# Kernel optimization log

Hardware: AMD Instinct MI355X
Metric: run time of the kernel (lower is better)

Reference implementation:

```python
import jax, jax.numpy as jnp
import numpy as np

# Conv config matching init_kwargs
C_IN, C_OUT = 128, 256
KH, KW = 3, 3
STRIDE = (1, 1)
PADDING = ((1, 1), (1, 1))
DILATION = (1, 1)
B, H, W = 32, 56, 56


def setup_inputs() -> dict:
    key = jax.random.key(0)
    k1, k2, k3 = jax.random.split(key, 3)
    x = jax.random.normal(k1, (B, C_IN, H, W), dtype=jnp.float32)
    # Flattened weight as stored by Conv2DUF: conv.weight.view(O,-1).t() -> [C*kh*kw, O]
    weight = jax.random.normal(k2, (C_IN * KH * KW, C_OUT), dtype=jnp.float32) * 0.02
    bias = jax.random.normal(k3, (C_OUT,), dtype=jnp.float32) * 0.02
    return {"x": x, "weight": weight, "bias": bias}


def reference(x, weight, bias):
    # Conv2DUF computes unfold(x) @ weight + bias, which is exactly a 2D
    # cross-correlation with the original conv kernel. Recover the [O,C,kh,kw]
    # kernel from the flattened [C*kh*kw, O] matrix and use the fused conv
    # primitive (same math, no giant im2col buffer).
    kernel = weight.T.reshape(C_OUT, C_IN, KH, KW)
    out = jax.lax.conv_general_dilated(
        x, kernel,
        window_strides=STRIDE,
        padding=PADDING,
        rhs_dilation=DILATION,
        dimension_numbers=("NCHW", "OIHW", "NCHW"),
    )
    return out + bias[None, :, None, None]
```

## Files before the change

### kernel.cpp

```cpp
#include <hip/hip_runtime.h>
#include <stdint.h>


#define C_INQ 128
#define C_OUTQ 256
#define HDIM 56
#define WDIM 56
#define BDIM 32
#define HP 58
#define WP 58
#define HWPIX (HDIM * WDIM)
#define GSTRIDE (BDIM * HP * WP * 8)
#define XT_ELEMS ((size_t)16 * GSTRIDE)
#define XT_BYTES (XT_ELEMS * 2)

typedef __bf16 bf16x8 __attribute__((ext_vector_type(8)));
typedef unsigned short ushort8 __attribute__((ext_vector_type(8)));
typedef float floatx4 __attribute__((ext_vector_type(4)));

__device__ __forceinline__ unsigned short f2bf(float f) {
  union { float f; unsigned int u; } v; v.f = f;
  unsigned int u = v.u;
  unsigned int r = u + 0x7FFFu + ((u >> 16) & 1u);
  return (unsigned short)(r >> 16);
}
__device__ __forceinline__ unsigned int pack2(float a, float b) {
  return (unsigned int)f2bf(a) | ((unsigned int)f2bf(b) << 16);
}

#define PAD_BLOCKS (BDIM * HP)
__global__ __launch_bounds__(256) void prep_kernel(
    const float* __restrict__ x, unsigned short* __restrict__ xt,
    const float* __restrict__ w, unsigned short* __restrict__ wt) {
  const int t = threadIdx.x;
  if (blockIdx.x < PAD_BLOCKS) {
    const int blk = blockIdx.x;
    const int b = blk / HP;
    const int hp = blk - b * HP;
    uint4* __restrict__ xt4 = (uint4*)xt;
    if (hp == 0 || hp == HP - 1) {
      for (int i = t; i < 16 * WP; i += 256) {
        int g = i / WP, wp = i - g * WP;
        xt4[((size_t)(g * BDIM + b) * HP + hp) * WP + wp] = make_uint4(0, 0, 0, 0);
      }
      return;
    }
    const int h = hp - 1;
    if (t < 224) {
      const int g = t / 14;
      const int w4 = (t - g * 14) * 4;
      const float* xp = x + ((size_t)b * C_INQ + g * 8) * HWPIX + h * WDIM + w4;
      float4 L0 = *(const float4*)(xp);
      float4 L1 = *(const float4*)(xp + HWPIX);
      float4 L2 = *(const float4*)(xp + 2 * HWPIX);
      float4 L3 = *(const float4*)(xp + 3 * HWPIX);
      float4 L4 = *(const float4*)(xp + 4 * HWPIX);
      float4 L5 = *(const float4*)(xp + 5 * HWPIX);
      float4 L6 = *(const float4*)(xp + 6 * HWPIX);
      float4 L7 = *(const float4*)(xp + 7 * HWPIX);
      uint4* dst = xt4 + ((size_t)(g * BDIM + b) * HP + hp) * WP + 1 + w4;
      dst[0] = make_uint4(pack2(L0.x, L1.x), pack2(L2.x, L3.x),
                          pack2(L4.x, L5.x), pack2(L6.x, L7.x));
      dst[1] = make_uint4(pack2(L0.y, L1.y), pack2(L2.y, L3.y),
                          pack2(L4.y, L5.y), pack2(L6.y, L7.y));
      dst[2] = make_uint4(pack2(L0.z, L1.z), pack2(L2.z, L3.z),
                          pack2(L4.z, L5.z), pack2(L6.z, L7.z));
      dst[3] = make_uint4(pack2(L0.w, L1.w), pack2(L2.w, L3.w),
                          pack2(L4.w, L5.w), pack2(L6.w, L7.w));
    } else {
      const int r = t - 224;
      const int g = r >> 1;
      const int wp = (r & 1) * (WP - 1);
      xt4[((size_t)(g * BDIM + b) * HP + hp) * WP + wp] = make_uint4(0, 0, 0, 0);
    }
  } else {
    const int bx = blockIdx.x - PAD_BLOCKS;
    const int khw = bx >> 4;
    const int r4 = bx & 15;
    const int n0w = (r4 >> 2) * 64;
    const int c32 = (r4 & 3) * 32;
    __shared__ float lds[32 * 66];
#pragma unroll
    for (int r = 0; r < 8; ++r) {
      int idx = r * 256 + t;
      int n = idx & 63, c = idx >> 6;
      lds[c * 66 + n] = w[(size_t)((c32 + c) * 9 + khw) * C_OUTQ + n0w + n];
    }
    __syncthreads();
    {
      int n = t >> 2, c8 = (t & 3) * 8;
      const float* s = lds + c8 * 66 + n;
      uint4 o;
      o.x = pack2(s[0],   s[66]);
      o.y = pack2(s[132], s[198]);
      o.z = pack2(s[264], s[330]);
      o.w = pack2(s[396], s[462]);
      *(uint4*)(wt + (size_t)khw * (C_OUTQ * C_INQ) + (size_t)(n0w + n) * C_INQ + c32 + c8) = o;
    }
  }
}

#define BM 256
#define BN 256
#define BK 64
#define NT 18

__global__ __launch_bounds__(512, 2) void conv_gemm_kernel(
    const unsigned short* __restrict__ xt,
    const unsigned short* __restrict__ wt,
    const float* __restrict__ bias,
    float* __restrict__ out) {
  __shared__ __align__(16) unsigned short ldsA[2 * BM * BK];
  __shared__ __align__(16) unsigned short ldsB[2 * BN * BK];

  const int t = threadIdx.x;
  const int lane = t & 63;
  const int wave = t >> 6;
  const int tile_m = blockIdx.x;

  int gbaseA[4], gbaseB[4];
#pragma unroll
  for (int r = 0; r < 4; ++r) {
    int g = r * 512 + t;
    int row = g >> 3;
    int kpart = (g & 7) ^ (row & 7);
    int pix = tile_m * BM + row;
    int b = pix / HWPIX;
    int p = pix - b * HWPIX;
    int h = p / WDIM;
    int w = p - h * WDIM;
    gbaseA[r] = kpart * GSTRIDE + ((b * HP + h) * WP + w) * 8;
  }
#pragma unroll
  for (int r = 0; r < 4; ++r) {
    int g = r * 512 + t;
    int n = g >> 3;
    int kpart = (g & 7) ^ (n & 7);
    gbaseB[r] = n * C_INQ + kpart * 8;
  }

  const int wm = (wave >> 2) * 128;
  const int wn = (wave & 3) * 64;
  const int mrow = lane & 15;
  const int quad = lane >> 4;
  const int xorv = mrow & 7;
  const int kx0 = (quad ^ xorv) * 8;
  const int kx1 = ((4 + quad) ^ xorv) * 8;

  floatx4 acc[8][4] = {};

  auto stage = [&](int kt, int buf) {
    const int khw = kt >> 1;
    const int chalf = kt & 1;
    const int kh = khw / 3;
    const int kw = khw - kh * 3;
    const int koffA = chalf * 8 * GSTRIDE + (kh * WP + kw) * 8;
    const int koffB = khw * (C_OUTQ * C_INQ) + chalf * 64;
    const int ldst = t * 8;
#pragma unroll
    for (int r = 0; r < 4; ++r)
      __builtin_amdgcn_global_load_lds(
          (const __attribute__((address_space(1))) unsigned int*)(xt + gbaseA[r] + koffA),
          (__attribute__((address_space(3))) unsigned int*)(ldsA + buf * (BM * BK) + r * 4096 + ldst),
          16, 0, 0);
#pragma unroll
    for (int r = 0; r < 4; ++r)
      __builtin_amdgcn_global_load_lds(
          (const __attribute__((address_space(1))) unsigned int*)(wt + gbaseB[r] + koffB),
          (__attribute__((address_space(3))) unsigned int*)(ldsB + buf * (BN * BK) + r * 4096 + ldst),
          16, 0, 0);
  };

  auto compute_tile = [&](int buf) {
    const unsigned short* A = ldsA + buf * (BM * BK);
    const unsigned short* B = ldsB + buf * (BN * BK);
    bf16x8 bfr[4][2];
#pragma unroll
    for (int j = 0; j < 4; ++j) {
      const unsigned short* br = B + (wn + j * 16 + mrow) * BK;
      bfr[j][0] = __builtin_bit_cast(bf16x8, *(const ushort8*)(br + kx0));
      bfr[j][1] = __builtin_bit_cast(bf16x8, *(const ushort8*)(br + kx1));
    }
#pragma unroll
    for (int p = 0; p < 4; ++p) {
      bf16x8 af[2][2];
#pragma unroll
      for (int i2 = 0; i2 < 2; ++i2) {
        const unsigned short* ar = A + (wm + (p * 2 + i2) * 16 + mrow) * BK;
        af[i2][0] = __builtin_bit_cast(bf16x8, *(const ushort8*)(ar + kx0));
        af[i2][1] = __builtin_bit_cast(bf16x8, *(const ushort8*)(ar + kx1));
      }
      __builtin_amdgcn_s_setprio(1);
#pragma unroll
      for (int i2 = 0; i2 < 2; ++i2)
#pragma unroll
        for (int u = 0; u < 2; ++u)
#pragma unroll
          for (int j = 0; j < 4; ++j)
            acc[p * 2 + i2][j] = __builtin_amdgcn_mfma_f32_16x16x32_bf16(
                af[i2][u], bfr[j][u], acc[p * 2 + i2][j], 0, 0, 0);
      __builtin_amdgcn_s_setprio(0);
    }
  };

#define K_STEP(T, BUF, VM, DOSTAGE)                                  \
  {                                                                  \
    asm volatile("s_waitcnt vmcnt(" VM ")" ::: "memory");            \
    __builtin_amdgcn_s_barrier();                                    \
    compute_tile(BUF);                                               \
    __builtin_amdgcn_s_barrier();                                    \
    if (DOSTAGE) stage((T) + 2, BUF);                                \
  }

  stage(0, 0);
  stage(1, 1);

#pragma unroll 1
  for (int tt = 0; tt < 16; tt += 2) {
    K_STEP(tt, 0, "8", true);
    K_STEP(tt + 1, 1, "8", true);
  }
  K_STEP(16, 0, "8", false);
  K_STEP(17, 1, "0", false);
#undef K_STEP

  float bv[4];
#pragma unroll
  for (int j = 0; j < 4; ++j) bv[j] = bias[wn + j * 16 + mrow];
#pragma unroll
  for (int i = 0; i < 8; ++i) {
    const int mbase = tile_m * BM + wm + i * 16 + quad * 4;
    const int b = mbase / HWPIX;
    const int p = mbase - b * HWPIX;
    float* obase = out + (size_t)b * (C_OUTQ * HWPIX) + p;
#pragma unroll
    for (int j = 0; j < 4; ++j) {
      const int ng = wn + j * 16 + mrow;
      floatx4 v = acc[i][j];
      v[0] += bv[j]; v[1] += bv[j]; v[2] += bv[j]; v[3] += bv[j];
      *(floatx4*)(obase + (size_t)ng * HWPIX) = v;
    }
  }
}

extern "C" void kernel_launch(void* const* d_in, const int* in_sizes, int n_in,
                              void* d_out, int out_size, void* d_ws, size_t ws_size,
                              hipStream_t stream) {
  const float* x    = (const float*)d_in[0];
  const float* w    = (const float*)d_in[1];
  const float* bias = (const float*)d_in[2];
  float* out = (float*)d_out;

  unsigned short* xt = (unsigned short*)d_ws;
  unsigned short* wt = (unsigned short*)((char*)d_ws + XT_BYTES);

  hipLaunchKernelGGL(prep_kernel, dim3(PAD_BLOCKS + 144), dim3(256), 0, stream,
                     x, xt, w, wt);
  hipLaunchKernelGGL(conv_gemm_kernel, dim3(392), dim3(512), 0, stream,
                     xt, wt, bias, out);
}
```

Before: 232.1 us.

## Rewrite conv GEMM with 128x256 tiles, 32x32 MFMA, single-buffered LDS

The GEMM kernel is restructured to use 128x256 block tiles with 256 threads and 32x32x16 bf16 MFMA instead of 16x16x32, doubling the grid to 784 blocks. Double-buffered LDS with explicit vmcnt pipelining is replaced by a single buffer synchronised with __syncthreads each K step. Block indices are remapped to interleave tiles. The aim is more blocks for occupancy and fewer MFMA instructions, at the cost of losing the load/compute overlap that double buffering gave.

```diff
diff --git a/kernel.cpp b/kernel.cpp
--- a/kernel.cpp
+++ b/kernel.cpp
@@ -17,6 +17,7 @@
 typedef __bf16 bf16x8 __attribute__((ext_vector_type(8)));
 typedef unsigned short ushort8 __attribute__((ext_vector_type(8)));
 typedef float floatx4 __attribute__((ext_vector_type(4)));
+typedef float floatx16 __attribute__((ext_vector_type(16)));
 
 __device__ __forceinline__ unsigned short f2bf(float f) {
   union { float f; unsigned int u; } v; v.f = f;
@@ -100,145 +101,120 @@
   }
 }
 
-#define BM 256
+#define BM 128
 #define BN 256
 #define BK 64
-#define NT 18
-
-__global__ __launch_bounds__(512, 2) void conv_gemm_kernel(
+#define STEPS 18
+
+__global__ __launch_bounds__(256, 2) void conv_gemm_kernel(
     const unsigned short* __restrict__ xt,
     const unsigned short* __restrict__ wt,
     const float* __restrict__ bias,
     float* __restrict__ out) {
-  __shared__ __align__(16) unsigned short ldsA[2 * BM * BK];
-  __shared__ __align__(16) unsigned short ldsB[2 * BN * BK];
+  __shared__ __align__(16) unsigned short ldsA[BM * BK];
+  __shared__ __align__(16) unsigned short ldsB[BN * BK];
 
   const int t = threadIdx.x;
   const int lane = t & 63;
   const int wave = t >> 6;
-  const int tile_m = blockIdx.x;
-
-  int gbaseA[4], gbaseB[4];
+  const int tile_m = ((int)blockIdx.x & 7) * 98 + ((int)blockIdx.x >> 3);
+
+  int gbaseA[4], gbaseB[8];
 #pragma unroll
   for (int r = 0; r < 4; ++r) {
-    int g = r * 512 + t;
+    int g = r * 256 + t;
     int row = g >> 3;
-    int kpart = (g & 7) ^ (row & 7);
+    int kp = (g & 7) ^ (row & 7);
     int pix = tile_m * BM + row;
     int b = pix / HWPIX;
     int p = pix - b * HWPIX;
     int h = p / WDIM;
     int w = p - h * WDIM;
-    gbaseA[r] = kpart * GSTRIDE + ((b * HP + h) * WP + w) * 8;
-  }
-#pragma unroll
-  for (int r = 0; r < 4; ++r) {
-    int g = r * 512 + t;
-    int n = g >> 3;
-    int kpart = (g & 7) ^ (n & 7);
-    gbaseB[r] = n * C_INQ + kpart * 8;
-  }
-
-  const int wm = (wave >> 2) * 128;
-  const int wn = (wave & 3) * 64;
-  const int mrow = lane & 15;
-  const int quad = lane >> 4;
-  const int xorv = mrow & 7;
-  const int kx0 = (quad ^ xorv) * 8;
-  const int kx1 = ((4 + quad) ^ xorv) * 8;
-
-  floatx4 acc[8][4] = {};
-
-  auto stage = [&](int kt, int buf) {
-    const int khw = kt >> 1;
-    const int chalf = kt & 1;
+    gbaseA[r] = kp * GSTRIDE + ((b * HP + h) * WP + w) * 8;
+  }
+#pragma unroll
+  for (int r = 0; r < 8; ++r) {
+    int g = r * 256 + t;
+    int row = g >> 3;
+    int kp = (g & 7) ^ (row & 7);
+    gbaseB[r] = row * C_INQ + kp * 8;
+  }
+
+  const int wm = (wave >> 1) * 64;
+  const int wn = (wave & 1) * 128;
+  const int l31 = lane & 31;
+  const int khalf = lane >> 5;
+
+  int arow[2], brow[4], sk[4];
+#pragma unroll
+  for (int mt = 0; mt < 2; ++mt) arow[mt] = (wm + mt * 32 + l31) * BK;
+#pragma unroll
+  for (int nt = 0; nt < 4; ++nt) brow[nt] = (wn + nt * 32 + l31) * BK;
+#pragma unroll
+  for (int ks = 0; ks < 4; ++ks) sk[ks] = ((2 * ks + khalf) ^ (l31 & 7)) * 8;
+
+  floatx16 acc[2][4] = {};
+
+#define BC8(p) __builtin_bit_cast(bf16x8, *(const ushort8*)(p))
+
+#pragma unroll 1
+  for (int s = 0; s < STEPS; ++s) {
+    const int khw = s >> 1;
+    const int ch = s & 1;
     const int kh = khw / 3;
     const int kw = khw - kh * 3;
-    const int koffA = chalf * 8 * GSTRIDE + (kh * WP + kw) * 8;
-    const int koffB = khw * (C_OUTQ * C_INQ) + chalf * 64;
-    const int ldst = t * 8;
+    const int koffA = ch * 8 * GSTRIDE + (kh * WP + kw) * 8;
+    const int koffB = khw * (C_OUTQ * C_INQ) + ch * 64;
 #pragma unroll
     for (int r = 0; r < 4; ++r)
       __builtin_amdgcn_global_load_lds(
           (const __attribute__((address_space(1))) unsigned int*)(xt + gbaseA[r] + koffA),
-          (__attribute__((address_space(3))) unsigned int*)(ldsA + buf * (BM * BK) + r * 4096 + ldst),
+          (__attribute__((address_space(3))) unsigned int*)(ldsA + (r * 256 + wave * 64) * 8),
           16, 0, 0);
 #pragma unroll
-    for (int r = 0; r < 4; ++r)
+    for (int r = 0; r < 8; ++r)
       __builtin_amdgcn_global_load_lds(
           (const __attribute__((address_space(1))) unsigned int*)(wt + gbaseB[r] + koffB),
-          (__attribute__((address_space(3))) unsigned int*)(ldsB + buf * (BN * BK) + r * 4096 + ldst),
+          (__attribute__((address_space(3))) unsigned int*)(ldsB + (r * 256 + wave * 64) * 8),
           16, 0, 0);
-  };
-
-  auto compute_tile = [&](int buf) {
-    const unsigned short* A = ldsA + buf * (BM * BK);
-    const unsigned short* B = ldsB + buf * (BN * BK);
-    bf16x8 bfr[4][2];
-#pragma unroll
-    for (int j = 0; j < 4; ++j) {
-      const unsigned short* br = B + (wn + j * 16 + mrow) * BK;
-      bfr[j][0] = __builtin_bit_cast(bf16x8, *(const ushort8*)(br + kx0));
-      bfr[j][1] = __builtin_bit_cast(bf16x8, *(const ushort8*)(br + kx1));
-    }
-#pragma unroll
-    for (int p = 0; p < 4; ++p) {
-      bf16x8 af[2][2];
-#pragma unroll
-      for (int i2 = 0; i2 < 2; ++i2) {
-        const unsigned short* ar = A + (wm + (p * 2 + i2) * 16 + mrow) * BK;
-        af[i2][0] = __builtin_bit_cast(bf16x8, *(const ushort8*)(ar + kx0));
-        af[i2][1] = __builtin_bit_cast(bf16x8, *(const ushort8*)(ar + kx1));
+    __syncthreads();
+
+#pragma unroll
+    for (int ks = 0; ks < 4; ++ks) {
+      bf16x8 a0 = BC8(ldsA + arow[0] + sk[ks]);
+      bf16x8 a1 = BC8(ldsA + arow[1] + sk[ks]);
+#pragma unroll
+      for (int nt = 0; nt < 4; ++nt) {
+        bf16x8 bfr = BC8(ldsB + brow[nt] + sk[ks]);
+        acc[0][nt] = __builtin_amdgcn_mfma_f32_32x32x16_bf16(a0, bfr, acc[0][nt], 0, 0, 0);
+        acc[1][nt] = __builtin_amdgcn_mfma_f32_32x32x16_bf16(a1, bfr, acc[1][nt], 0, 0, 0);
       }
-      __builtin_amdgcn_s_setprio(1);
-#pragma unroll
-      for (int i2 = 0; i2 < 2; ++i2)
-#pragma unroll
-        for (int u = 0; u < 2; ++u)
-#pragma unroll
-          for (int j = 0; j < 4; ++j)
-            acc[p * 2 + i2][j] = __builtin_amdgcn_mfma_f32_16x16x32_bf16(
-                af[i2][u], bfr[j][u], acc[p * 2 + i2][j], 0, 0, 0);
-      __builtin_amdgcn_s_setprio(0);
-    }
-  };
-
-#define K_STEP(T, BUF, VM, DOSTAGE)                                  \
-  {                                                                  \
-    asm volatile("s_waitcnt vmcnt(" VM ")" ::: "memory");            \
-    __builtin_amdgcn_s_barrier();                                    \
-    compute_tile(BUF);                                               \
-    __builtin_amdgcn_s_barrier();                                    \
-    if (DOSTAGE) stage((T) + 2, BUF);                                \
-  }
-
-  stage(0, 0);
-  stage(1, 1);
-
-#pragma unroll 1
-  for (int tt = 0; tt < 16; tt += 2) {
-    K_STEP(tt, 0, "8", true);
-    K_STEP(tt + 1, 1, "8", true);
-  }
-  K_STEP(16, 0, "8", false);
-  K_STEP(17, 1, "0", false);
-#undef K_STEP
+    }
+    __syncthreads();
+  }
+#undef BC8
 
   float bv[4];
 #pragma unroll
-  for (int j = 0; j < 4; ++j) bv[j] = bias[wn + j * 16 + mrow];
-#pragma unroll
-  for (int i = 0; i < 8; ++i) {
-    const int mbase = tile_m * BM + wm + i * 16 + quad * 4;
-    const int b = mbase / HWPIX;
-    const int p = mbase - b * HWPIX;
-    float* obase = out + (size_t)b * (C_OUTQ * HWPIX) + p;
-#pragma unroll
-    for (int j = 0; j < 4; ++j) {
-      const int ng = wn + j * 16 + mrow;
-      floatx4 v = acc[i][j];
-      v[0] += bv[j]; v[1] += bv[j]; v[2] += bv[j]; v[3] += bv[j];
-      *(floatx4*)(obase + (size_t)ng * HWPIX) = v;
+  for (int nt = 0; nt < 4; ++nt) bv[nt] = bias[wn + nt * 32 + l31];
+#pragma unroll
+  for (int mt = 0; mt < 2; ++mt) {
+#pragma unroll
+    for (int g = 0; g < 4; ++g) {
+      const int mbase = tile_m * BM + wm + mt * 32 + g * 8 + khalf * 4;
+      const int b = mbase / HWPIX;
+      const int p = mbase - b * HWPIX;
+      float* obase = out + (size_t)b * (C_OUTQ * HWPIX) + p;
+#pragma unroll
+      for (int nt = 0; nt < 4; ++nt) {
+        const int n = wn + nt * 32 + l31;
+        floatx4 v;
+        v[0] = acc[mt][nt][g * 4 + 0] + bv[nt];
+        v[1] = acc[mt][nt][g * 4 + 1] + bv[nt];
+        v[2] = acc[mt][nt][g * 4 + 2] + bv[nt];
+        v[3] = acc[mt][nt][g * 4 + 3] + bv[nt];
+        *(floatx4*)(obase + (size_t)n * HWPIX) = v;
+      }
     }
   }
 }
@@ -256,6 +232,6 @@
 
   hipLaunchKernelGGL(prep_kernel, dim3(PAD_BLOCKS + 144), dim3(256), 0, stream,
                      x, xt, w, wt);
-  hipLaunchKernelGGL(conv_gemm_kernel, dim3(392), dim3(512), 0, stream,
+  hipLaunchKernelGGL(conv_gemm_kernel, dim3(784), dim3(256), 0, stream,
                      xt, wt, bias, out);
 }
```

Result: no change. 236.5 us (+1.9%).
